# Kernel optimization log

Measured on AMD Instinct MI355X. Metric: run time of the kernel, lower is better.

## Reference

```python
import jax, jax.numpy as jnp
import numpy as np

B, H, S, D = 2, 16, 4096, 128


def setup_inputs() -> dict:
    key = jax.random.key(0)
    kq, kk, kv = jax.random.split(key, 3)
    q = jax.random.normal(kq, (B, H, S, D), dtype=jnp.float32)
    k = jax.random.normal(kk, (B, H, S, D), dtype=jnp.float32)
    v = jax.random.normal(kv, (B, H, S, D), dtype=jnp.float32)
    return {"q": q, "k": k, "v": v}


def reference(q, k, v):
    # kv: [B,H,D,D] = k^T @ v (contract over sequence)
    kv = jnp.einsum("bhsd,bhse->bhde", k, v)
    # out: v + q @ kv  -> [B,H,S,D]
    return v + jnp.einsum("bhsd,bhde->bhse", q, kv)
```

## Files before the change

kernel.cpp:

```cpp
#include <hip/hip_runtime.h>
#include <hip/hip_bf16.h>

#define BHN 32
#define SEQ 4096
#define DIM 128
#define TROWS 64

typedef __bf16 bf16x8 __attribute__((ext_vector_type(8)));
typedef __bf16 bf16x4 __attribute__((ext_vector_type(4)));
typedef float  f32x4  __attribute__((ext_vector_type(4)));

__device__ __forceinline__ bf16x8 cvt8(const float* f) {
    bf16x8 r;
#pragma unroll
    for (int i = 0; i < 8; ++i) r[i] = (__bf16)f[i];
    return r;
}

template<int CH>
__global__ __launch_bounds__(512) void p1_kv(const float* __restrict__ kin,
                                             const float* __restrict__ vin,
                                             __bf16* __restrict__ ws1) {
    constexpr int SR = SEQ / CH;
    constexpr int NT = SR / TROWS;

    __shared__ __align__(16) __bf16 kt[DIM][TROWS];
    __shared__ __align__(16) __bf16 vt[DIM][TROWS];

    const int bh    = blockIdx.x / CH;
    const int chunk = blockIdx.x % CH;
    const int tid = threadIdx.x;

    const int dcol = tid & 31;
    const int sgrp = tid >> 5;
    const int d0 = dcol * 4;
    const int s0 = sgrp * 4;

    const int w = tid >> 6;
    const int l = tid & 63;
    const int g = l >> 4;
    const int c = l & 15;

    const float* kb = kin + (size_t)bh * SEQ * DIM + (size_t)chunk * SR * DIM;
    const float* vb = vin + (size_t)bh * SEQ * DIM + (size_t)chunk * SR * DIM;

    f32x4 acc[8];
#pragma unroll
    for (int nt = 0; nt < 8; ++nt) acc[nt] = (f32x4){0.f, 0.f, 0.f, 0.f};

    for (int t = 0; t < NT; ++t) {
        const float* kp = kb + (size_t)(t * TROWS + s0) * DIM + d0;
        const float* vp = vb + (size_t)(t * TROWS + s0) * DIM + d0;
        f32x4 kr[4], vr[4];
#pragma unroll
        for (int j = 0; j < 4; ++j) {
            kr[j] = *(const f32x4*)(kp + j * DIM);
            vr[j] = *(const f32x4*)(vp + j * DIM);
        }
#pragma unroll
        for (int jd = 0; jd < 4; ++jd) {
            const int dd  = d0 + jd;
            const int key = (dd & 7) ^ ((dd >> 2) & 7);
            const int off = (((sgrp >> 1) ^ key) * 8) + (sgrp & 1) * 4;
            bf16x4 pk, pv;
#pragma unroll
            for (int j = 0; j < 4; ++j) {
                pk[j] = (__bf16)kr[j][jd];
                pv[j] = (__bf16)vr[j][jd];
            }
            *(bf16x4*)&kt[dd][off] = pk;
            *(bf16x4*)&vt[dd][off] = pv;
        }
        __syncthreads();

        const int e    = w * 16 + c;
        const int keyE = (e & 7) ^ ((e >> 2) & 7);
#pragma unroll
        for (int st = 0; st < 2; ++st) {
            bf16x8 af = *(const bf16x8*)&vt[e][((st * 4 + g) ^ keyE) * 8];
#pragma unroll
            for (int nt = 0; nt < 8; ++nt) {
                const int d    = nt * 16 + c;
                const int keyD = (d & 7) ^ ((d >> 2) & 7);
                bf16x8 bfr = *(const bf16x8*)&kt[d][((st * 4 + g) ^ keyD) * 8];
                acc[nt] = __builtin_amdgcn_mfma_f32_16x16x32_bf16(af, bfr, acc[nt], 0, 0, 0);
            }
        }
        __syncthreads();
    }

    __bf16* outp = ws1 + ((size_t)chunk * BHN + bh) * (DIM * DIM);
#pragma unroll
    for (int nt = 0; nt < 8; ++nt) {
        bf16x4 p;
#pragma unroll
        for (int r = 0; r < 4; ++r) p[r] = (__bf16)acc[nt][r];
        *(bf16x4*)(outp + nt * 2048 + tid * 4) = p;
    }
}

template<int CH>
__global__ __launch_bounds__(256) void p1_reduce(const __bf16* __restrict__ ws1,
                                                 __bf16* __restrict__ ws2) {
    const int t   = blockIdx.x * 256 + threadIdx.x;
    const int bh  = t >> 11;
    const int r11 = t & 2047;

    const __bf16* base = ws1 + (size_t)bh * (DIM * DIM) + r11 * 8;
    float s[8] = {0.f, 0.f, 0.f, 0.f, 0.f, 0.f, 0.f, 0.f};
#pragma unroll
    for (int ch = 0; ch < CH; ++ch) {
        bf16x8 a = *(const bf16x8*)(base + (size_t)ch * BHN * DIM * DIM);
#pragma unroll
        for (int i = 0; i < 8; ++i) s[i] += (float)a[i];
    }

    __bf16* dst = ws2 + (size_t)bh * (DIM * DIM);
#pragma unroll
    for (int i = 0; i < 8; ++i) {
        const int f  = r11 * 8 + i;
        const int nt = f >> 11;
        const int wv = (f >> 8) & 7;
        const int gg = (f >> 6) & 3;
        const int cc = (f >> 2) & 15;
        const int r  = f & 3;
        const int e  = wv * 16 + gg * 4 + r;
        const int d  = nt * 16 + cc;
        dst[e * DIM + (((d >> 3) ^ (e & 15)) * 8) + (d & 7)] = (__bf16)s[i];
    }
}

__global__ __launch_bounds__(512) void p2_qkv(const float* __restrict__ qin,
                                              const float* __restrict__ vin,
                                              const __bf16* __restrict__ ws2,
                                              float* __restrict__ outp) {
    __shared__ __align__(16) __bf16 kvs[DIM * DIM];

    const int bh = blockIdx.x & 31;
    const int rc = blockIdx.x >> 5;
    const int tid = threadIdx.x;

    {
        const uint4* src = (const uint4*)(ws2 + (size_t)bh * DIM * DIM);
        uint4* dst = (uint4*)kvs;
#pragma unroll
        for (int j = 0; j < 4; ++j) dst[tid + j * 512] = src[tid + j * 512];
    }
    __syncthreads();

    const int w = tid >> 6;
    const int l = tid & 63;
    const int g = l >> 4;
    const int c = l & 15;
    const int s = rc * 128 + w * 16 + c;

    const float* qrow = qin + (size_t)bh * SEQ * DIM + (size_t)s * DIM + g * 8;
    bf16x8 bq[4];
#pragma unroll
    for (int ks = 0; ks < 4; ++ks) {
        f32x4 x = *(const f32x4*)(qrow + ks * 32);
        f32x4 y = *(const f32x4*)(qrow + ks * 32 + 4);
        float tmp[8];
        tmp[0]=x[0]; tmp[1]=x[1]; tmp[2]=x[2]; tmp[3]=x[3];
        tmp[4]=y[0]; tmp[5]=y[1]; tmp[6]=y[2]; tmp[7]=y[3];
        bq[ks] = cvt8(tmp);
    }

    f32x4 acc[8];
#pragma unroll
    for (int et = 0; et < 8; ++et) acc[et] = (f32x4){0.f, 0.f, 0.f, 0.f};

#pragma unroll
    for (int ks = 0; ks < 4; ++ks) {
#pragma unroll
        for (int et = 0; et < 8; ++et) {
            const int e = et * 16 + c;
            const int slot = (ks * 4 + g) ^ c;
            bf16x8 a = *(const bf16x8*)&kvs[e * DIM + slot * 8];
            acc[et] = __builtin_amdgcn_mfma_f32_16x16x32_bf16(a, bq[ks], acc[et], 0, 0, 0);
        }
    }

    const float* vb = vin + (size_t)bh * SEQ * DIM;
    float* ob = outp + (size_t)bh * SEQ * DIM;
#pragma unroll
    for (int et = 0; et < 8; ++et) {
        const size_t idx = (size_t)s * DIM + et * 16 + g * 4;
        f32x4 vv = *(const f32x4*)(vb + idx);
        f32x4 o = acc[et] + vv;
        *(f32x4*)(ob + idx) = o;
    }
}

extern "C" void kernel_launch(void* const* d_in, const int* in_sizes, int n_in,
                              void* d_out, int out_size, void* d_ws, size_t ws_size,
                              hipStream_t stream) {
    const float* q = (const float*)d_in[0];
    const float* k = (const float*)d_in[1];
    const float* v = (const float*)d_in[2];
    float* out = (float*)d_out;

    __bf16* ws2 = (__bf16*)d_ws;
    __bf16* ws1 = (__bf16*)d_ws + (size_t)BHN * DIM * DIM;

    const size_t slab = (size_t)BHN * DIM * DIM * sizeof(__bf16);
    if (ws_size >= slab * (1 + 32)) {
        p1_kv<32><<<BHN * 32, 512, 0, stream>>>(k, v, ws1);
        p1_reduce<32><<<256, 256, 0, stream>>>(ws1, ws2);
    } else {
        p1_kv<16><<<BHN * 16, 512, 0, stream>>>(k, v, ws1);
        p1_reduce<16><<<256, 256, 0, stream>>>(ws1, ws2);
    }
    p2_qkv<<<BHN * (SEQ / 128), 512, 0, stream>>>(q, v, ws2, out);
}
```

Baseline: 77.76 us.

## Double-buffer K/V register loads, interleave chunk tiles, fix split at 16

Measured after the change: 68.41 us. 1.14x faster.

```diff
diff --git a/kernel.cpp b/kernel.cpp
--- a/kernel.cpp
+++ b/kernel.cpp
@@ -15,6 +15,15 @@
 #pragma unroll
     for (int i = 0; i < 8; ++i) r[i] = (__bf16)f[i];
     return r;
+}
+
+__device__ __forceinline__ void load8(const float* kp, const float* vp,
+                                      f32x4 kr[4], f32x4 vr[4]) {
+#pragma unroll
+    for (int j = 0; j < 4; ++j) {
+        kr[j] = *(const f32x4*)(kp + j * DIM);
+        vr[j] = *(const f32x4*)(vp + j * DIM);
+    }
 }
 
 template<int CH>
@@ -41,22 +50,29 @@
     const int g = l >> 4;
     const int c = l & 15;
 
-    const float* kb = kin + (size_t)bh * SEQ * DIM + (size_t)chunk * SR * DIM;
-    const float* vb = vin + (size_t)bh * SEQ * DIM + (size_t)chunk * SR * DIM;
+    const float* hk = kin + (size_t)bh * SEQ * DIM;
+    const float* hv = vin + (size_t)bh * SEQ * DIM;
 
     f32x4 acc[8];
 #pragma unroll
     for (int nt = 0; nt < 8; ++nt) acc[nt] = (f32x4){0.f, 0.f, 0.f, 0.f};
 
+    f32x4 kr[2][4], vr[2][4];
+    {
+        const size_t off = ((size_t)chunk * TROWS + s0) * DIM + d0;
+        load8(hk + off, hv + off, kr[0], vr[0]);
+    }
+
+#pragma unroll
     for (int t = 0; t < NT; ++t) {
-        const float* kp = kb + (size_t)(t * TROWS + s0) * DIM + d0;
-        const float* vp = vb + (size_t)(t * TROWS + s0) * DIM + d0;
-        f32x4 kr[4], vr[4];
-#pragma unroll
-        for (int j = 0; j < 4; ++j) {
-            kr[j] = *(const f32x4*)(kp + j * DIM);
-            vr[j] = *(const f32x4*)(vp + j * DIM);
-        }
+        const int cur = t & 1;
+
+        if (t + 1 < NT) {
+            const size_t off =
+                ((size_t)((t + 1) * CH + chunk) * TROWS + s0) * DIM + d0;
+            load8(hk + off, hv + off, kr[cur ^ 1], vr[cur ^ 1]);
+        }
+
 #pragma unroll
         for (int jd = 0; jd < 4; ++jd) {
             const int dd  = d0 + jd;
@@ -65,8 +81,8 @@
             bf16x4 pk, pv;
 #pragma unroll
             for (int j = 0; j < 4; ++j) {
-                pk[j] = (__bf16)kr[j][jd];
-                pv[j] = (__bf16)vr[j][jd];
+                pk[j] = (__bf16)kr[cur][j][jd];
+                pv[j] = (__bf16)vr[cur][j][jd];
             }
             *(bf16x4*)&kt[dd][off] = pk;
             *(bf16x4*)&vt[dd][off] = pv;
@@ -203,13 +219,7 @@
     __bf16* ws2 = (__bf16*)d_ws;
     __bf16* ws1 = (__bf16*)d_ws + (size_t)BHN * DIM * DIM;
 
-    const size_t slab = (size_t)BHN * DIM * DIM * sizeof(__bf16);
-    if (ws_size >= slab * (1 + 32)) {
-        p1_kv<32><<<BHN * 32, 512, 0, stream>>>(k, v, ws1);
-        p1_reduce<32><<<256, 256, 0, stream>>>(ws1, ws2);
-    } else {
-        p1_kv<16><<<BHN * 16, 512, 0, stream>>>(k, v, ws1);
-        p1_reduce<16><<<256, 256, 0, stream>>>(ws1, ws2);
-    }
+    p1_kv<16><<<BHN * 16, 512, 0, stream>>>(k, v, ws1);
+    p1_reduce<16><<<256, 256, 0, stream>>>(ws1, ws2);
     p2_qkv<<<BHN * (SEQ / 128), 512, 0, stream>>>(q, v, ws2, out);
 }
```

## Double-buffer K/V LDS tiles with register prefetch and fix chunk count at 16

Applied to the files above, without the earlier changes.

Result: faster. 68.97 us (-11.3%).

```diff
diff --git a/kernel.cpp b/kernel.cpp
--- a/kernel.cpp
+++ b/kernel.cpp
@@ -24,8 +24,8 @@
     constexpr int SR = SEQ / CH;
     constexpr int NT = SR / TROWS;
 
-    __shared__ __align__(16) __bf16 kt[DIM][TROWS];
-    __shared__ __align__(16) __bf16 vt[DIM][TROWS];
+    __shared__ __align__(16) __bf16 kt[2][DIM][TROWS];
+    __shared__ __align__(16) __bf16 vt[2][DIM][TROWS];
 
     const int bh    = blockIdx.x / CH;
     const int chunk = blockIdx.x % CH;
@@ -48,54 +48,71 @@
 #pragma unroll
     for (int nt = 0; nt < 8; ++nt) acc[nt] = (f32x4){0.f, 0.f, 0.f, 0.f};
 
+    f32x4 kr[4], vr[4];
+    {
+        const size_t off = (size_t)s0 * DIM + d0;
+#pragma unroll
+        for (int j = 0; j < 4; ++j) {
+            kr[j] = *(const f32x4*)(kb + off + j * DIM);
+            vr[j] = *(const f32x4*)(vb + off + j * DIM);
+        }
+    }
+
+#pragma unroll
     for (int t = 0; t < NT; ++t) {
-        const float* kp = kb + (size_t)(t * TROWS + s0) * DIM + d0;
-        const float* vp = vb + (size_t)(t * TROWS + s0) * DIM + d0;
-        f32x4 kr[4], vr[4];
-#pragma unroll
-        for (int j = 0; j < 4; ++j) {
-            kr[j] = *(const f32x4*)(kp + j * DIM);
-            vr[j] = *(const f32x4*)(vp + j * DIM);
-        }
+        const int p = t & 1;
+
 #pragma unroll
         for (int jd = 0; jd < 4; ++jd) {
             const int dd  = d0 + jd;
             const int key = (dd & 7) ^ ((dd >> 2) & 7);
-            const int off = (((sgrp >> 1) ^ key) * 8) + (sgrp & 1) * 4;
+            const int o   = (((sgrp >> 1) ^ key) * 8) + (sgrp & 1) * 4;
             bf16x4 pk, pv;
 #pragma unroll
             for (int j = 0; j < 4; ++j) {
                 pk[j] = (__bf16)kr[j][jd];
                 pv[j] = (__bf16)vr[j][jd];
             }
-            *(bf16x4*)&kt[dd][off] = pk;
-            *(bf16x4*)&vt[dd][off] = pv;
-        }
-        __syncthreads();
+            *(bf16x4*)&kt[p][dd][o] = pk;
+            *(bf16x4*)&vt[p][dd][o] = pv;
+        }
+
+        __builtin_amdgcn_sched_barrier(0);
+        if (t + 1 < NT) {
+            const size_t off = ((size_t)((t + 1) * TROWS + s0)) * DIM + d0;
+#pragma unroll
+            for (int j = 0; j < 4; ++j) {
+                kr[j] = *(const f32x4*)(kb + off + j * DIM);
+                vr[j] = *(const f32x4*)(vb + off + j * DIM);
+            }
+        }
+        __builtin_amdgcn_sched_barrier(0);
+
+        asm volatile("s_waitcnt lgkmcnt(0)" ::: "memory");
+        __builtin_amdgcn_s_barrier();
 
         const int e    = w * 16 + c;
         const int keyE = (e & 7) ^ ((e >> 2) & 7);
 #pragma unroll
         for (int st = 0; st < 2; ++st) {
-            bf16x8 af = *(const bf16x8*)&vt[e][((st * 4 + g) ^ keyE) * 8];
+            bf16x8 af = *(const bf16x8*)&vt[p][e][((st * 4 + g) ^ keyE) * 8];
 #pragma unroll
             for (int nt = 0; nt < 8; ++nt) {
                 const int d    = nt * 16 + c;
                 const int keyD = (d & 7) ^ ((d >> 2) & 7);
-                bf16x8 bfr = *(const bf16x8*)&kt[d][((st * 4 + g) ^ keyD) * 8];
+                bf16x8 bfr = *(const bf16x8*)&kt[p][d][((st * 4 + g) ^ keyD) * 8];
                 acc[nt] = __builtin_amdgcn_mfma_f32_16x16x32_bf16(af, bfr, acc[nt], 0, 0, 0);
             }
         }
-        __syncthreads();
     }
 
     __bf16* outp = ws1 + ((size_t)chunk * BHN + bh) * (DIM * DIM);
 #pragma unroll
     for (int nt = 0; nt < 8; ++nt) {
-        bf16x4 p;
-#pragma unroll
-        for (int r = 0; r < 4; ++r) p[r] = (__bf16)acc[nt][r];
-        *(bf16x4*)(outp + nt * 2048 + tid * 4) = p;
+        bf16x4 pq;
+#pragma unroll
+        for (int r = 0; r < 4; ++r) pq[r] = (__bf16)acc[nt][r];
+        *(bf16x4*)(outp + nt * 2048 + tid * 4) = pq;
     }
 }
 
@@ -203,13 +220,7 @@
     __bf16* ws2 = (__bf16*)d_ws;
     __bf16* ws1 = (__bf16*)d_ws + (size_t)BHN * DIM * DIM;
 
-    const size_t slab = (size_t)BHN * DIM * DIM * sizeof(__bf16);
-    if (ws_size >= slab * (1 + 32)) {
-        p1_kv<32><<<BHN * 32, 512, 0, stream>>>(k, v, ws1);
-        p1_reduce<32><<<256, 256, 0, stream>>>(ws1, ws2);
-    } else {
-        p1_kv<16><<<BHN * 16, 512, 0, stream>>>(k, v, ws1);
-        p1_reduce<16><<<256, 256, 0, stream>>>(ws1, ws2);
-    }
+    p1_kv<16><<<BHN * 16, 512, 0, stream>>>(k, v, ws1);
+    p1_reduce<16><<<256, 256, 0, stream>>>(ws1, ws2);
     p2_qkv<<<BHN * (SEQ / 128), 512, 0, stream>>>(q, v, ws2, out);
 }
```
